# Performance work log

Measured on AMD Instinct MI355X. Metric: run time of the kernel, lower is better.

Reference implementation:

```python
import jax, jax.numpy as jnp
import numpy as np
import math

FREQS = jnp.array([1., 2., 4., 8., 7., 5.], dtype=jnp.float32)  # default frequencies


def setup_inputs() -> dict:
    key = jax.random.key(0)
    k1, k2, k3 = jax.random.split(key, 3)
    B, N, H, F = 8, 4096, 256, 6
    x = jax.random.normal(k1, (B, N, H), dtype=jnp.float32)
    t = jax.random.uniform(k2, (B, 1), dtype=jnp.float32) * (2.0 * math.pi)
    oscillators = jax.random.normal(k3, (F, H, H), dtype=jnp.float32) * 0.1
    # phase_shifts[i] = i / F * pi, broadcast over hidden dim (matches torch init)
    phase_shifts = jnp.broadcast_to(
        (jnp.arange(F, dtype=jnp.float32) / F * math.pi)[:, None], (F, H)
    ).copy()
    return {"x": x, "t": t, "oscillators": oscillators, "phase_shifts": phase_shifts}


def reference(x, t, oscillators, phase_shifts):
    # resonator[b, f, h] = sin(freq_f * t[b, 0] + phase[f, h])
    res = jnp.sin(FREQS[None, :, None] * t[:, :, None] + phase_shifts[None, :, :])  # [B, F, H]
    # result[b, n, k] = sum_f (x[b, n, :] @ W_f)[k] * res[b, f, k]
    return jnp.einsum('bnh,fhk,bfk->bnk', x, oscillators, res)
```

## Files before the change

### kernel.cpp

```cpp
#include <hip/hip_runtime.h>
#include <hip/hip_bf16.h>


#define B_  8
#define N_  4096
#define H_  256

typedef __attribute__((ext_vector_type(8))) short s8v;
typedef __attribute__((ext_vector_type(4))) float f4v;

__global__ __launch_bounds__(256) void build_w(
    const float* __restrict__ osc,
    const float* __restrict__ t,
    const float* __restrict__ phase,
    __hip_bfloat16* __restrict__ Wt)
{
    const float freqs[6] = {1.f, 2.f, 4.f, 8.f, 7.f, 5.f};
    int idx = blockIdx.x * 256 + threadIdx.x;
    int b   = idx >> 16;
    int rem = idx & 65535;
    int n   = rem >> 8;
    int h   = rem & 255;
    float tb  = t[b];
    float acc = 0.f;
#pragma unroll
    for (int f = 0; f < 6; ++f) {
        float s = __sinf(freqs[f] * tb + phase[f * 256 + n]);
        acc += osc[f * 65536 + h * 256 + n] * s;
    }
    Wt[idx] = __float2bfloat16(acc);
}

#define LDSTRIDE 40

__global__ __launch_bounds__(256) void gemm(
    const float* __restrict__ X,
    const __hip_bfloat16* __restrict__ Wt,
    float* __restrict__ out)
{
    __shared__ short As[128 * LDSTRIDE];
    __shared__ short Bs[128 * LDSTRIDE];

    const int b     = blockIdx.z;
    const int mTile = blockIdx.y;
    const int nTile = blockIdx.x;

    const int tid    = threadIdx.x;
    const int lane   = tid & 63;
    const int wave   = tid >> 6;
    const int lane15 = lane & 15;
    const int quad   = lane >> 4;
    const int wm     = wave >> 1;
    const int wn     = wave & 1;

    const float* Xb          = X   + (size_t)b * N_ * H_ + (size_t)mTile * 128 * H_;
    const __hip_bfloat16* Wb = Wt  + (size_t)b * H_ * H_ + (size_t)nTile * 128 * H_;
    float* Ob                = out + (size_t)b * N_ * H_ + (size_t)mTile * 128 * H_ + nTile * 128;

    const int sm = tid >> 1;
    const int sh = tid & 1;

    f4v acc[4][4] = {};

    for (int k0 = 0; k0 < H_; k0 += 32) {
        const float4* pa = (const float4*)(Xb + (size_t)sm * H_ + k0 + sh * 16);
        float4 a0 = pa[0], a1 = pa[1], a2 = pa[2], a3 = pa[3];
        union { __hip_bfloat162 h[8]; uint4 q[2]; } cv;
        cv.h[0] = __float22bfloat162_rn(make_float2(a0.x, a0.y));
        cv.h[1] = __float22bfloat162_rn(make_float2(a0.z, a0.w));
        cv.h[2] = __float22bfloat162_rn(make_float2(a1.x, a1.y));
        cv.h[3] = __float22bfloat162_rn(make_float2(a1.z, a1.w));
        cv.h[4] = __float22bfloat162_rn(make_float2(a2.x, a2.y));
        cv.h[5] = __float22bfloat162_rn(make_float2(a2.z, a2.w));
        cv.h[6] = __float22bfloat162_rn(make_float2(a3.x, a3.y));
        cv.h[7] = __float22bfloat162_rn(make_float2(a3.z, a3.w));
        *(uint4*)(&As[sm * LDSTRIDE + sh * 16 + 0]) = cv.q[0];
        *(uint4*)(&As[sm * LDSTRIDE + sh * 16 + 8]) = cv.q[1];

        const uint4* pb = (const uint4*)(Wb + (size_t)sm * H_ + k0 + sh * 16);
        uint4 b0 = pb[0], b1 = pb[1];
        *(uint4*)(&Bs[sm * LDSTRIDE + sh * 16 + 0]) = b0;
        *(uint4*)(&Bs[sm * LDSTRIDE + sh * 16 + 8]) = b1;
        __syncthreads();

        s8v af[4], bf[4];
#pragma unroll
        for (int mt = 0; mt < 4; ++mt)
            af[mt] = *(const s8v*)(&As[(wm * 64 + mt * 16 + lane15) * LDSTRIDE + quad * 8]);
#pragma unroll
        for (int nt = 0; nt < 4; ++nt)
            bf[nt] = *(const s8v*)(&Bs[(wn * 64 + nt * 16 + lane15) * LDSTRIDE + quad * 8]);

#pragma unroll
        for (int mt = 0; mt < 4; ++mt)
#pragma unroll
            for (int nt = 0; nt < 4; ++nt)
                acc[mt][nt] = __builtin_amdgcn_mfma_f32_16x16x32_bf16(
                    af[mt], bf[nt], acc[mt][nt], 0, 0, 0);
        __syncthreads();
    }

#pragma unroll
    for (int mt = 0; mt < 4; ++mt) {
#pragma unroll
        for (int r = 0; r < 4; ++r) {
            int row = wm * 64 + mt * 16 + quad * 4 + r;
            float* po = Ob + (size_t)row * H_ + wn * 64 + lane15;
#pragma unroll
            for (int nt = 0; nt < 4; ++nt)
                po[nt * 16] = acc[mt][nt][r];
        }
    }
}

extern "C" void kernel_launch(void* const* d_in, const int* in_sizes, int n_in,
                              void* d_out, int out_size, void* d_ws, size_t ws_size,
                              hipStream_t stream) {
    const float* x     = (const float*)d_in[0];
    const float* t     = (const float*)d_in[1];
    const float* osc   = (const float*)d_in[2];
    const float* phase = (const float*)d_in[3];
    __hip_bfloat16* Wt = (__hip_bfloat16*)d_ws;
    float* out = (float*)d_out;

    build_w<<<2048, 256, 0, stream>>>(osc, t, phase, Wt);

    dim3 grid(2, 32, 8);
    gemm<<<grid, 256, 0, stream>>>(x, Wt, out);
}
```

Measured before the change: 109.7 us.

## Use 512-thread GEMM blocks with register prefetch of next K slice

```diff
diff --git a/kernel.cpp b/kernel.cpp
--- a/kernel.cpp
+++ b/kernel.cpp
@@ -33,7 +33,7 @@
 
 #define LDSTRIDE 40
 
-__global__ __launch_bounds__(256) void gemm(
+__global__ __launch_bounds__(512) void gemm(
     const float* __restrict__ X,
     const __hip_bfloat16* __restrict__ Wt,
     float* __restrict__ out)
@@ -42,8 +42,8 @@
     __shared__ short Bs[128 * LDSTRIDE];
 
     const int b     = blockIdx.z;
-    const int mTile = blockIdx.y;
-    const int nTile = blockIdx.x;
+    const int mTile = blockIdx.x;
+    const int nTile = blockIdx.y;
 
     const int tid    = threadIdx.x;
     const int lane   = tid & 63;
@@ -57,42 +57,45 @@
     const __hip_bfloat16* Wb = Wt  + (size_t)b * H_ * H_ + (size_t)nTile * 128 * H_;
     float* Ob                = out + (size_t)b * N_ * H_ + (size_t)mTile * 128 * H_ + nTile * 128;
 
-    const int sm = tid >> 1;
-    const int sh = tid & 1;
+    const int srow = tid >> 2;
+    const int skq  = tid & 3;
 
-    f4v acc[4][4] = {};
+    const float* pa          = Xb + (size_t)srow * H_ + skq * 8;
+    const __hip_bfloat16* pb = Wb + (size_t)srow * H_ + skq * 8;
 
-    for (int k0 = 0; k0 < H_; k0 += 32) {
-        const float4* pa = (const float4*)(Xb + (size_t)sm * H_ + k0 + sh * 16);
-        float4 a0 = pa[0], a1 = pa[1], a2 = pa[2], a3 = pa[3];
-        union { __hip_bfloat162 h[8]; uint4 q[2]; } cv;
+    f4v acc[2][4] = {};
+
+    float4 a0 = *(const float4*)(pa);
+    float4 a1 = *(const float4*)(pa + 4);
+    uint4  bv = *(const uint4*)(pb);
+
+    for (int it = 0; it < 8; ++it) {
+        union { __hip_bfloat162 h[4]; uint4 q; } cv;
         cv.h[0] = __float22bfloat162_rn(make_float2(a0.x, a0.y));
         cv.h[1] = __float22bfloat162_rn(make_float2(a0.z, a0.w));
         cv.h[2] = __float22bfloat162_rn(make_float2(a1.x, a1.y));
         cv.h[3] = __float22bfloat162_rn(make_float2(a1.z, a1.w));
-        cv.h[4] = __float22bfloat162_rn(make_float2(a2.x, a2.y));
-        cv.h[5] = __float22bfloat162_rn(make_float2(a2.z, a2.w));
-        cv.h[6] = __float22bfloat162_rn(make_float2(a3.x, a3.y));
-        cv.h[7] = __float22bfloat162_rn(make_float2(a3.z, a3.w));
-        *(uint4*)(&As[sm * LDSTRIDE + sh * 16 + 0]) = cv.q[0];
-        *(uint4*)(&As[sm * LDSTRIDE + sh * 16 + 8]) = cv.q[1];
-
-        const uint4* pb = (const uint4*)(Wb + (size_t)sm * H_ + k0 + sh * 16);
-        uint4 b0 = pb[0], b1 = pb[1];
-        *(uint4*)(&Bs[sm * LDSTRIDE + sh * 16 + 0]) = b0;
-        *(uint4*)(&Bs[sm * LDSTRIDE + sh * 16 + 8]) = b1;
+        *(uint4*)(&As[srow * LDSTRIDE + skq * 8]) = cv.q;
+        *(uint4*)(&Bs[srow * LDSTRIDE + skq * 8]) = bv;
         __syncthreads();
 
-        s8v af[4], bf[4];
+        if (it < 7) {
+            const float4* na          = (const float4*)(pa + (it + 1) * 32);
+            a0 = na[0];
+            a1 = na[1];
+            bv = *(const uint4*)(pb + (it + 1) * 32);
+        }
+
+        s8v af[2], bf[4];
 #pragma unroll
-        for (int mt = 0; mt < 4; ++mt)
-            af[mt] = *(const s8v*)(&As[(wm * 64 + mt * 16 + lane15) * LDSTRIDE + quad * 8]);
+        for (int mt = 0; mt < 2; ++mt)
+            af[mt] = *(const s8v*)(&As[(wm * 32 + mt * 16 + lane15) * LDSTRIDE + quad * 8]);
 #pragma unroll
         for (int nt = 0; nt < 4; ++nt)
             bf[nt] = *(const s8v*)(&Bs[(wn * 64 + nt * 16 + lane15) * LDSTRIDE + quad * 8]);
 
 #pragma unroll
-        for (int mt = 0; mt < 4; ++mt)
+        for (int mt = 0; mt < 2; ++mt)
 #pragma unroll
             for (int nt = 0; nt < 4; ++nt)
                 acc[mt][nt] = __builtin_amdgcn_mfma_f32_16x16x32_bf16(
@@ -101,10 +104,10 @@
     }
 
 #pragma unroll
-    for (int mt = 0; mt < 4; ++mt) {
+    for (int mt = 0; mt < 2; ++mt) {
 #pragma unroll
         for (int r = 0; r < 4; ++r) {
-            int row = wm * 64 + mt * 16 + quad * 4 + r;
+            int row = wm * 32 + mt * 16 + quad * 4 + r;
             float* po = Ob + (size_t)row * H_ + wn * 64 + lane15;
 #pragma unroll
             for (int nt = 0; nt < 4; ++nt)
@@ -125,6 +128,6 @@
 
     build_w<<<2048, 256, 0, stream>>>(osc, t, phase, Wt);
 
-    dim3 grid(2, 32, 8);
-    gemm<<<grid, 256, 0, stream>>>(x, Wt, out);
+    dim3 grid(32, 2, 8);
+    gemm<<<grid, 512, 0, stream>>>(x, Wt, out);
 }
```

Result: no change. 109.7 us (-0.1%).
